# Performance work log

Hardware: AMD Instinct MI355X
Metric: run time of the kernel (lower is better)

Reference implementation:

```python
import jax, jax.numpy as jnp
import numpy as np

N_NODES = 100_000
N_EDGES = 50_000
D_FEAT = 128
N_LAYERS = 2
HID = 256          # 2*dim in the out head
N_CLASS = 40
M_N2E = 800_000    # node-in-hyperedge incidences
M_E2N = 800_000    # hyperedge-at-node incidences


def _seg_mean(x, seg, num_segments):
    # global_mean_pool: scatter-mean over segment ids
    s = jax.ops.segment_sum(x, seg, num_segments=num_segments)
    c = jax.ops.segment_sum(jnp.ones((x.shape[0], 1), x.dtype), seg, num_segments=num_segments)
    return s / jnp.maximum(c, 1.0)


def setup_inputs() -> dict:
    key = jax.random.key(0)
    ks = jax.random.split(key, 6)
    node_x = jax.random.normal(ks[0], (N_NODES, D_FEAT), jnp.float32)
    nodes_map = jax.random.randint(ks[1], (M_N2E,), 0, N_NODES)
    # segment ids: every hyperedge gets M_N2E//N_EDGES members (sorted, no empty segments)
    edge_batch = jnp.arange(M_N2E, dtype=jnp.int32) // (M_N2E // N_EDGES)
    edges_map = jax.random.randint(ks[2], (M_E2N,), 0, N_EDGES)
    node_batch = jnp.arange(M_E2N, dtype=jnp.int32) // (M_E2N // N_NODES)
    d_final = D_FEAT * (2 ** N_LAYERS)  # feature dim doubles each layer via concat
    W1 = jax.random.normal(ks[3], (d_final, HID), jnp.float32) * 0.02
    b1 = jnp.zeros((HID,), jnp.float32)
    W2 = jax.random.normal(ks[4], (HID, N_CLASS), jnp.float32) * 0.02
    b2 = jnp.zeros((N_CLASS,), jnp.float32)
    return {"node_x": node_x, "nodes_map": nodes_map, "edge_batch": edge_batch,
            "edges_map": edges_map, "node_batch": node_batch,
            "W1": W1, "b1": b1, "W2": W2, "b2": b2}


def reference(node_x, nodes_map, edge_batch, edges_map, node_batch, W1, b1, W2, b2):
    # Inference mode: dropout is identity; convs=False so GCN subnets are skipped.
    for _ in range(N_LAYERS):
        xs = node_x
        # N2E: gather node features into hyperedge incidence rows, mean-pool per hyperedge
        edge_x = jax.nn.relu(_seg_mean(node_x[nodes_map], edge_batch, N_EDGES))
        # E2N: gather hyperedge features at node incidence rows, mean-pool per node
        nx = jax.nn.relu(_seg_mean(edge_x[edges_map], node_batch, N_NODES))
        node_x = jnp.concatenate([xs, nx], axis=1)
    h = jax.nn.relu(node_x @ W1 + b1)
    return jax.nn.log_softmax(h @ W2 + b2, axis=-1)
```

## Files before the change

### kernel.cpp

```cpp
#include <hip/hip_runtime.h>
#include <hip/hip_bf16.h>

typedef unsigned int u32;
typedef unsigned short u16;
typedef unsigned char u8;
typedef __attribute__((ext_vector_type(4))) float f32x4;
typedef __attribute__((ext_vector_type(2))) float f32x2;

#define N_NODES 100000
#define N_EDGES 50000
#define D0      128
#define MPAD    100096
#define HIDN    256
#define NC      40

__device__ __forceinline__ float b2f(u32 h) { return __uint_as_float(h << 16); }
__device__ __forceinline__ u16 f2b(float f) {
  u32 u = __float_as_uint(f);
  u32 r = (u + 0x7fffu + ((u >> 16) & 1u)) >> 16;
  return (u16)r;
}
__device__ __forceinline__ void load_lds16(const void* g, void* l) {
  __builtin_amdgcn_global_load_lds((const __attribute__((address_space(1))) u32*)g,
                                   (__attribute__((address_space(3))) u32*)l, 16, 0, 0);
}


__global__ __launch_bounds__(256) void k_node_to_x0f(const float* __restrict__ x, u8* __restrict__ x0f) {
  int t = blockIdx.x * 256 + threadIdx.x;
  const float4 v = *(const float4*)(x + (size_t)t * 4);
  int w = __builtin_amdgcn_cvt_pk_fp8_f32(v.x, v.y, 0, false);
  w = __builtin_amdgcn_cvt_pk_fp8_f32(v.z, v.w, w, true);
  *(u32*)(x0f + (size_t)t * 4) = (u32)w;
}

__global__ __launch_bounds__(256) void k_padf(u8* __restrict__ x0f, u8* __restrict__ nx1f,
                                              u8* __restrict__ nx2f) {
  int t = blockIdx.x * 256 + threadIdx.x;
  const size_t PO = (size_t)N_NODES * D0;
  u32* dst;
  if (t < 3072)      dst = (u32*)(x0f + PO) + t;
  else if (t < 6144) dst = (u32*)(nx1f + PO) + (t - 3072);
  else               dst = (u32*)(nx2f + PO) + (t - 6144);
  *dst = 0;
}

__global__ __launch_bounds__(192) void k_w1ff(const float* __restrict__ W1, u8* __restrict__ W1F) {
  int n = blockIdx.x;
  int t = threadIdx.x;
  float v[2];
#pragma unroll
  for (int j = 0; j < 2; ++j) {
    int k = 2 * t + j;
    if (k < 128)      v[j] = W1[k * 256 + n];
    else if (k < 256) v[j] = W1[k * 256 + n] + W1[(k + 128) * 256 + n];
    else              v[j] = W1[(k + 128) * 256 + n];
  }
  int w = __builtin_amdgcn_cvt_pk_fp8_f32(v[0] * 64.f, v[1] * 64.f, 0, false);
  *(u16*)(W1F + (size_t)n * 384 + 2 * t) = (u16)w;
}

__global__ __launch_bounds__(256) void k_w2t(const float* __restrict__ W2, u16* __restrict__ W2T) {
  int t = blockIdx.x * 256 + threadIdx.x;
  int n = t >> 8, k = t & 255;
  W2T[t] = (n < NC) ? f2b(W2[k * NC + n]) : (u16)0;
}


template<int DEG>
__global__ __launch_bounds__(256) void k_gatherf(const u8* __restrict__ src,
                                                 const int* __restrict__ map,
                                                 u8* __restrict__ dst) {
  int gw = (blockIdx.x * 256 + threadIdx.x) >> 6;
  int lane = threadIdx.x & 63;
  int my = (lane < DEG) ? map[gw * DEG + lane] : 0;
  float a0 = 0.f, a1 = 0.f;
#pragma unroll
  for (int r = 0; r < DEG; ++r) {
    int idx = __shfl(my, r);
    u16 h = *(const u16*)(src + (size_t)idx * D0 + lane * 2);
    f32x2 v = __builtin_amdgcn_cvt_pk_f32_fp8((int)h, false);
    a0 += v[0]; a1 += v[1];
  }
  const float s = 1.f / DEG;
  int w = __builtin_amdgcn_cvt_pk_fp8_f32(fmaxf(a0 * s, 0.f), fmaxf(a1 * s, 0.f), 0, false);
  *(u16*)(dst + (size_t)gw * D0 + lane * 2) = (u16)w;
}

__global__ __launch_bounds__(256) void k_head(const u8* __restrict__ x0f,
                                              const u8* __restrict__ nx1f,
                                              const u8* __restrict__ nx2f,
                                              const u8* __restrict__ W1F,
                                              const float* __restrict__ b1,
                                              const u16* __restrict__ W2T,
                                              const float* __restrict__ b2,
                                              float* __restrict__ out) {
  __shared__ char lds[40960];
  u8*  As = (u8*)lds;
  u8*  Bs = (u8*)(lds + 8192);
  u16* Hs = (u16*)lds;
  const int tid = threadIdx.x;
  const int lane = tid & 63;
  const int wid = tid >> 6;
  const int m0 = blockIdx.x * 64;

  f32x4 acc[4][4] = {};

#pragma unroll
  for (int ks = 0; ks < 3; ++ks) {
    const u8* Ap = (ks == 0) ? x0f : (ks == 1) ? nx1f : nx2f;
    __syncthreads();
    const int c = tid & 7;
#pragma unroll
    for (int p = 0; p < 2; ++p) {
      int row = p * 32 + (tid >> 3);
      load_lds16(Ap + (size_t)(m0 + row) * D0 + ((c ^ (row & 7)) << 4),
                 (char*)As + (p * 256 + tid) * 16);
    }
#pragma unroll
    for (int p = 0; p < 8; ++p) {
      int row = p * 32 + (tid >> 3);
      load_lds16(W1F + (size_t)row * 384 + ks * 128 + ((c ^ (row & 7)) << 4),
                 (char*)Bs + (p * 256 + tid) * 16);
    }
    __syncthreads();
#pragma unroll
    for (int kk = 0; kk < 4; ++kk) {
      long av[4], bv[4];
#pragma unroll
      for (int m = 0; m < 4; ++m) {
        int r = m * 16 + (lane & 15);
        int byo = (kk * 32 + ((lane >> 4) * 8)) ^ ((r & 7) << 4);
        av[m] = *(const long*)(As + r * 128 + byo);
      }
#pragma unroll
      for (int n = 0; n < 4; ++n) {
        int r = wid * 64 + n * 16 + (lane & 15);
        int byo = (kk * 32 + ((lane >> 4) * 8)) ^ ((r & 7) << 4);
        bv[n] = *(const long*)(Bs + r * 128 + byo);
      }
#pragma unroll
      for (int m = 0; m < 4; ++m)
#pragma unroll
        for (int n = 0; n < 4; ++n)
          acc[m][n] = __builtin_amdgcn_mfma_f32_16x16x32_fp8_fp8(av[m], bv[n], acc[m][n], 0, 0, 0);
    }
  }

  __syncthreads();
  const int rb = (lane >> 4) * 4, cb = lane & 15;
#pragma unroll
  for (int n = 0; n < 4; ++n) {
    int col = wid * 64 + n * 16 + cb;
    float bv = b1[col];
#pragma unroll
    for (int m = 0; m < 4; ++m) {
#pragma unroll
      for (int v = 0; v < 4; ++v) {
        int r = m * 16 + rb + v;
        u32 byo = ((u32)(r << 9) + (u32)(col << 1)) ^ (u32)((r & 7) << 4);
        *(u16*)((char*)Hs + byo) = f2b(fmaxf(acc[m][n][v] * 0.015625f + bv, 0.f));
      }
    }
  }
  __syncthreads();

  typedef __attribute__((ext_vector_type(8))) short bf16x8;
  f32x4 acc2[3] = {};
  const int r0g = wid * 16;
#pragma unroll
  for (int kk = 0; kk < 8; ++kk) {
    int arow = r0g + (lane & 15);
    int kb = (kk * 64 + ((lane >> 4) * 16)) ^ ((arow & 7) << 4);
    bf16x8 a = *(const bf16x8*)((const char*)Hs + arow * 512 + kb);
#pragma unroll
    for (int n = 0; n < 3; ++n) {
      int brow = n * 16 + (lane & 15);
      bf16x8 b = *(const bf16x8*)(W2T + brow * 256 + kk * 32 + (lane >> 4) * 8);
      acc2[n] = __builtin_amdgcn_mfma_f32_16x16x32_bf16(a, b, acc2[n], 0, 0, 0);
    }
  }

  float bias[3];
#pragma unroll
  for (int n = 0; n < 3; ++n) {
    int c2 = n * 16 + cb;
    bias[n] = (c2 < NC) ? b2[c2] : 0.f;
  }
#pragma unroll
  for (int v = 0; v < 4; ++v) {
    float z[3];
    float mx = -1e30f;
#pragma unroll
    for (int n = 0; n < 3; ++n) {
      int c2 = n * 16 + cb;
      z[n] = (c2 < NC) ? (acc2[n][v] + bias[n]) : -1e30f;
      mx = fmaxf(mx, z[n]);
    }
#pragma unroll
    for (int o = 1; o < 16; o <<= 1) mx = fmaxf(mx, __shfl_xor(mx, o));
    float s = 0.f;
#pragma unroll
    for (int n = 0; n < 3; ++n) {
      int c2 = n * 16 + cb;
      if (c2 < NC) s += expf(z[n] - mx);
    }
#pragma unroll
    for (int o = 1; o < 16; o <<= 1) s += __shfl_xor(s, o);
    float lse = logf(s);
    int grow = m0 + r0g + rb + v;
    if (grow < N_NODES) {
#pragma unroll
      for (int n = 0; n < 3; ++n) {
        int c2 = n * 16 + cb;
        if (c2 < NC) out[(size_t)grow * NC + c2] = z[n] - mx - lse;
      }
    }
  }
}


extern "C" void kernel_launch(void* const* d_in, const int* in_sizes, int n_in,
                              void* d_out, int out_size, void* d_ws, size_t ws_size,
                              hipStream_t stream) {
  const float* node_x    = (const float*)d_in[0];
  const int*   nodes_map = (const int*)d_in[1];
  const int*   edges_map = (const int*)d_in[3];
  const float* W1        = (const float*)d_in[5];
  const float* b1        = (const float*)d_in[6];
  const float* W2        = (const float*)d_in[7];
  const float* b2        = (const float*)d_in[8];
  float* out = (float*)d_out;
  char* ws = (char*)d_ws;

  u8*  x0f  = (u8*)(ws + 0);
  u8*  nx1f = (u8*)(ws + 12812288);
  u8*  nx2f = (u8*)(ws + 25624576);
  u8*  E1f  = (u8*)(ws + 38436864);
  u8*  E2f  = (u8*)(ws + 44836864);
  u8*  W1F  = (u8*)(ws + 51236864);
  u16* W2T  = (u16*)(ws + 51335168);

  k_node_to_x0f<<<12500, 256, 0, stream>>>(node_x, x0f);
  k_padf<<<36, 256, 0, stream>>>(x0f, nx1f, nx2f);
  k_w1ff<<<256, 192, 0, stream>>>(W1, W1F);
  k_w2t<<<48, 256, 0, stream>>>(W2, W2T);

  k_gatherf<16><<<N_EDGES / 4, 256, 0, stream>>>(x0f, nodes_map, E1f);
  k_gatherf<8><<<N_NODES / 4, 256, 0, stream>>>(E1f, edges_map, nx1f);
  k_gatherf<16><<<N_EDGES / 4, 256, 0, stream>>>(nx1f, nodes_map, E2f);
  k_gatherf<8><<<N_NODES / 4, 256, 0, stream>>>(E2f, edges_map, nx2f);

  k_head<<<MPAD / 64, 256, 0, stream>>>(x0f, nx1f, nx2f, W1F, b1, W2T, b2, out);
}
```

Baseline: 218.7 us.

## Fuse prep kernels and widen gathers to 16-byte loads with permuted feature layout

Merges the four small preprocessing kernels into one launch. The gather kernel now reads whole 16-byte chunks per lane, with each wave handling two segments, and reduces the partial sums across lane groups with shuffles. The head GEMM loads 16 bytes per LDS read and issues two MFMAs per read. This works because the feature columns of x0f and W1F are stored in a consistent permuted order. The aim is fewer, wider memory transactions and less launch overhead, at the cost of more shuffle reductions and register pressure in the gather.

Measured after the change: 308.3 us. +41.0%, slower.

```diff
diff --git a/kernel.cpp b/kernel.cpp
--- a/kernel.cpp
+++ b/kernel.cpp
@@ -6,6 +6,7 @@
 typedef unsigned char u8;
 typedef __attribute__((ext_vector_type(4))) float f32x4;
 typedef __attribute__((ext_vector_type(2))) float f32x2;
+typedef __attribute__((ext_vector_type(2))) long i64x2;
 
 #define N_NODES 100000
 #define N_EDGES 50000
@@ -24,67 +25,115 @@
   __builtin_amdgcn_global_load_lds((const __attribute__((address_space(1))) u32*)g,
                                    (__attribute__((address_space(3))) u32*)l, 16, 0, 0);
 }
-
-
-__global__ __launch_bounds__(256) void k_node_to_x0f(const float* __restrict__ x, u8* __restrict__ x0f) {
-  int t = blockIdx.x * 256 + threadIdx.x;
-  const float4 v = *(const float4*)(x + (size_t)t * 4);
-  int w = __builtin_amdgcn_cvt_pk_fp8_f32(v.x, v.y, 0, false);
-  w = __builtin_amdgcn_cvt_pk_fp8_f32(v.z, v.w, w, true);
-  *(u32*)(x0f + (size_t)t * 4) = (u32)w;
-}
-
-__global__ __launch_bounds__(256) void k_padf(u8* __restrict__ x0f, u8* __restrict__ nx1f,
-                                              u8* __restrict__ nx2f) {
-  int t = blockIdx.x * 256 + threadIdx.x;
-  const size_t PO = (size_t)N_NODES * D0;
-  u32* dst;
-  if (t < 3072)      dst = (u32*)(x0f + PO) + t;
-  else if (t < 6144) dst = (u32*)(nx1f + PO) + (t - 3072);
-  else               dst = (u32*)(nx2f + PO) + (t - 6144);
-  *dst = 0;
-}
-
-__global__ __launch_bounds__(192) void k_w1ff(const float* __restrict__ W1, u8* __restrict__ W1F) {
-  int n = blockIdx.x;
-  int t = threadIdx.x;
-  float v[2];
-#pragma unroll
-  for (int j = 0; j < 2; ++j) {
-    int k = 2 * t + j;
-    if (k < 128)      v[j] = W1[k * 256 + n];
-    else if (k < 256) v[j] = W1[k * 256 + n] + W1[(k + 128) * 256 + n];
-    else              v[j] = W1[(k + 128) * 256 + n];
-  }
-  int w = __builtin_amdgcn_cvt_pk_fp8_f32(v[0] * 64.f, v[1] * 64.f, 0, false);
-  *(u16*)(W1F + (size_t)n * 384 + 2 * t) = (u16)w;
-}
-
-__global__ __launch_bounds__(256) void k_w2t(const float* __restrict__ W2, u16* __restrict__ W2T) {
-  int t = blockIdx.x * 256 + threadIdx.x;
-  int n = t >> 8, k = t & 255;
-  W2T[t] = (n < NC) ? f2b(W2[k * NC + n]) : (u16)0;
-}
-
+__device__ __forceinline__ int swapf(int o) {
+  return ((o >> 2) & 0x18) | ((o << 2) & 0x60) | (o & 7);
+}
+
+__global__ __launch_bounds__(256) void k_prep(const float* __restrict__ node_x,
+                                              const float* __restrict__ W1,
+                                              const float* __restrict__ W2,
+                                              u8* __restrict__ x0f, u8* __restrict__ nx1f,
+                                              u8* __restrict__ nx2f, u8* __restrict__ W1F,
+                                              u16* __restrict__ W2T) {
+  const int blk = blockIdx.x;
+  const int tid = threadIdx.x;
+  if (blk < 12500) {
+    int t = blk * 256 + tid;
+    int row = t >> 5;
+    int o = (t & 31) * 4;
+    int p = swapf(o);
+    const float4 v = *(const float4*)(node_x + (size_t)row * 128 + p);
+    int w = __builtin_amdgcn_cvt_pk_fp8_f32(v.x, v.y, 0, false);
+    w = __builtin_amdgcn_cvt_pk_fp8_f32(v.z, v.w, w, true);
+    *(u32*)(x0f + (size_t)row * 128 + o) = (u32)w;
+  } else if (blk < 12536) {
+    int t = (blk - 12500) * 256 + tid;
+    const size_t PO = (size_t)N_NODES * 128;
+    u32* dst;
+    if (t < 3072)      dst = (u32*)(x0f + PO) + t;
+    else if (t < 6144) dst = (u32*)(nx1f + PO) + (t - 3072);
+    else               dst = (u32*)(nx2f + PO) + (t - 6144);
+    *dst = 0;
+  } else if (blk < 12792) {
+    int n = blk - 12536;
+    if (tid < 192) {
+      int d0 = 2 * tid;
+      int c = d0 >> 7, od = d0 & 127;
+      int ks = (c << 7) | swapf(od);
+      float v[2];
+#pragma unroll
+      for (int j = 0; j < 2; ++j) {
+        int k = ks + j;
+        if (k < 128)      v[j] = W1[k * 256 + n];
+        else if (k < 256) v[j] = W1[k * 256 + n] + W1[(k + 128) * 256 + n];
+        else              v[j] = W1[(k + 128) * 256 + n];
+      }
+      int w = __builtin_amdgcn_cvt_pk_fp8_f32(v[0] * 64.f, v[1] * 64.f, 0, false);
+      *(u16*)(W1F + (size_t)n * 384 + d0) = (u16)w;
+    }
+  } else {
+    int t = (blk - 12792) * 256 + tid;
+    int n = t >> 8, k = t & 255;
+    W2T[t] = (n < NC) ? f2b(W2[k * NC + n]) : (u16)0;
+  }
+}
 
 template<int DEG>
 __global__ __launch_bounds__(256) void k_gatherf(const u8* __restrict__ src,
                                                  const int* __restrict__ map,
                                                  u8* __restrict__ dst) {
-  int gw = (blockIdx.x * 256 + threadIdx.x) >> 6;
-  int lane = threadIdx.x & 63;
-  int my = (lane < DEG) ? map[gw * DEG + lane] : 0;
-  float a0 = 0.f, a1 = 0.f;
-#pragma unroll
-  for (int r = 0; r < DEG; ++r) {
-    int idx = __shfl(my, r);
-    u16 h = *(const u16*)(src + (size_t)idx * D0 + lane * 2);
-    f32x2 v = __builtin_amdgcn_cvt_pk_f32_fp8((int)h, false);
-    a0 += v[0]; a1 += v[1];
+  const int wave = (blockIdx.x * 256 + threadIdx.x) >> 6;
+  const int lane = threadIdx.x & 63;
+  const int g = lane >> 3, b = lane & 7;
+  const int s0 = wave * 2;
+  constexpr int R = DEG / 8;
+  int mm = ((lane & 31) < DEG) ? map[(size_t)(s0 + (lane >> 5)) * DEG + (lane & 31)] : 0;
+  uint4 v[2][R];
+#pragma unroll
+  for (int si = 0; si < 2; ++si)
+#pragma unroll
+    for (int r = 0; r < R; ++r) {
+      int idx = __shfl(mm, si * 32 + r * 8 + g);
+      v[si][r] = *(const uint4*)(src + (size_t)idx * 128 + b * 16);
+    }
+  float acc[2][16];
+#pragma unroll
+  for (int si = 0; si < 2; ++si) {
+#pragma unroll
+    for (int j = 0; j < 16; ++j) acc[si][j] = 0.f;
+#pragma unroll
+    for (int r = 0; r < R; ++r) {
+      u32 w4[4] = {v[si][r].x, v[si][r].y, v[si][r].z, v[si][r].w};
+#pragma unroll
+      for (int c = 0; c < 4; ++c) {
+        f32x2 lo = __builtin_amdgcn_cvt_pk_f32_fp8((int)w4[c], false);
+        f32x2 hi = __builtin_amdgcn_cvt_pk_f32_fp8((int)w4[c], true);
+        acc[si][c * 4 + 0] += lo[0]; acc[si][c * 4 + 1] += lo[1];
+        acc[si][c * 4 + 2] += hi[0]; acc[si][c * 4 + 3] += hi[1];
+      }
+    }
+#pragma unroll
+    for (int st = 8; st < 64; st <<= 1)
+#pragma unroll
+      for (int j = 0; j < 16; ++j)
+        acc[si][j] += __shfl_xor(acc[si][j], st);
   }
   const float s = 1.f / DEG;
-  int w = __builtin_amdgcn_cvt_pk_fp8_f32(fmaxf(a0 * s, 0.f), fmaxf(a1 * s, 0.f), 0, false);
-  *(u16*)(dst + (size_t)gw * D0 + lane * 2) = (u16)w;
+  if (g < 2) {
+    u32 ww[4];
+#pragma unroll
+    for (int c = 0; c < 4; ++c) {
+      float a0 = (g == 0) ? acc[0][c * 4 + 0] : acc[1][c * 4 + 0];
+      float a1 = (g == 0) ? acc[0][c * 4 + 1] : acc[1][c * 4 + 1];
+      float a2 = (g == 0) ? acc[0][c * 4 + 2] : acc[1][c * 4 + 2];
+      float a3 = (g == 0) ? acc[0][c * 4 + 3] : acc[1][c * 4 + 3];
+      int w = __builtin_amdgcn_cvt_pk_fp8_f32(fmaxf(a0 * s, 0.f), fmaxf(a1 * s, 0.f), 0, false);
+      w = __builtin_amdgcn_cvt_pk_fp8_f32(fmaxf(a2 * s, 0.f), fmaxf(a3 * s, 0.f), w, true);
+      ww[c] = (u32)w;
+    }
+    uint4 o; o.x = ww[0]; o.y = ww[1]; o.z = ww[2]; o.w = ww[3];
+    *(uint4*)(dst + (size_t)(s0 + g) * 128 + b * 16) = o;
+  }
 }
 
 __global__ __launch_bounds__(256) void k_head(const u8* __restrict__ x0f,
@@ -103,6 +152,7 @@
   const int lane = tid & 63;
   const int wid = tid >> 6;
   const int m0 = blockIdx.x * 64;
+  const int q = lane >> 4;
 
   f32x4 acc[4][4] = {};
 
@@ -125,25 +175,27 @@
     }
     __syncthreads();
 #pragma unroll
-    for (int kk = 0; kk < 4; ++kk) {
-      long av[4], bv[4];
+    for (int h = 0; h < 2; ++h) {
+      long a0[4], a1[4], b0[4], b1[4];
 #pragma unroll
       for (int m = 0; m < 4; ++m) {
         int r = m * 16 + (lane & 15);
-        int byo = (kk * 32 + ((lane >> 4) * 8)) ^ ((r & 7) << 4);
-        av[m] = *(const long*)(As + r * 128 + byo);
+        i64x2 t = *(const i64x2*)(As + r * 128 + ((q * 32 + h * 16) ^ ((r & 7) << 4)));
+        a0[m] = t[0]; a1[m] = t[1];
       }
 #pragma unroll
       for (int n = 0; n < 4; ++n) {
         int r = wid * 64 + n * 16 + (lane & 15);
-        int byo = (kk * 32 + ((lane >> 4) * 8)) ^ ((r & 7) << 4);
-        bv[n] = *(const long*)(Bs + r * 128 + byo);
+        i64x2 t = *(const i64x2*)(Bs + r * 128 + ((q * 32 + h * 16) ^ ((r & 7) << 4)));
+        b0[n] = t[0]; b1[n] = t[1];
       }
 #pragma unroll
       for (int m = 0; m < 4; ++m)
 #pragma unroll
-        for (int n = 0; n < 4; ++n)
-          acc[m][n] = __builtin_amdgcn_mfma_f32_16x16x32_fp8_fp8(av[m], bv[n], acc[m][n], 0, 0, 0);
+        for (int n = 0; n < 4; ++n) {
+          acc[m][n] = __builtin_amdgcn_mfma_f32_16x16x32_fp8_fp8(a0[m], b0[n], acc[m][n], 0, 0, 0);
+          acc[m][n] = __builtin_amdgcn_mfma_f32_16x16x32_fp8_fp8(a1[m], b1[n], acc[m][n], 0, 0, 0);
+        }
     }
   }
 
@@ -241,15 +293,12 @@
   u8*  W1F  = (u8*)(ws + 51236864);
   u16* W2T  = (u16*)(ws + 51335168);
 
-  k_node_to_x0f<<<12500, 256, 0, stream>>>(node_x, x0f);
-  k_padf<<<36, 256, 0, stream>>>(x0f, nx1f, nx2f);
-  k_w1ff<<<256, 192, 0, stream>>>(W1, W1F);
-  k_w2t<<<48, 256, 0, stream>>>(W2, W2T);
-
-  k_gatherf<16><<<N_EDGES / 4, 256, 0, stream>>>(x0f, nodes_map, E1f);
-  k_gatherf<8><<<N_NODES / 4, 256, 0, stream>>>(E1f, edges_map, nx1f);
-  k_gatherf<16><<<N_EDGES / 4, 256, 0, stream>>>(nx1f, nodes_map, E2f);
-  k_gatherf<8><<<N_NODES / 4, 256, 0, stream>>>(E2f, edges_map, nx2f);
+  k_prep<<<12840, 256, 0, stream>>>(node_x, W1, W2, x0f, nx1f, nx2f, W1F, W2T);
+
+  k_gatherf<16><<<6250, 256, 0, stream>>>(x0f, nodes_map, E1f);
+  k_gatherf<8><<<12500, 256, 0, stream>>>(E1f, edges_map, nx1f);
+  k_gatherf<16><<<6250, 256, 0, stream>>>(nx1f, nodes_map, E2f);
+  k_gatherf<8><<<12500, 256, 0, stream>>>(E2f, edges_map, nx2f);
 
   k_head<<<MPAD / 64, 256, 0, stream>>>(x0f, nx1f, nx2f, W1F, b1, W2T, b2, out);
 }
```
